# Optimization experiments

Measured on AMD Instinct MI355X. Metric: run time of the kernel, lower is better.

## Reference

```python
import jax, jax.numpy as jnp
import numpy as np

B, N, E, H, NDIM, WS = 1, 4096, 512, 8, 16, 128


def setup_inputs() -> dict:
    key = jax.random.key(0)
    ks = jax.random.split(key, 8)
    x = jax.random.normal(ks[0], (B, N, E), jnp.float32)
    W_qkv = jax.random.normal(ks[1], (E, 3 * E), jnp.float32) * (E ** -0.5)
    b_qkv = jnp.zeros((3 * E,), jnp.float32)
    W_out = jax.random.normal(ks[2], (E, E), jnp.float32) * (E ** -0.5)
    b_out = jnp.zeros((E,), jnp.float32)
    omega = jax.random.normal(ks[3], (E,), jnp.float32)
    p_coeff = 0.1 * jax.random.normal(ks[4], (E, NDIM), jnp.float32)
    # keep |q|<1 so the 4096-step EMA recurrence is stable (original randn init diverges)
    q_coeff = jax.random.uniform(ks[5], (E, NDIM), jnp.float32, minval=-0.95, maxval=0.95)
    gamma = 0.1 * jax.random.normal(ks[6], (E, NDIM), jnp.float32)
    adaptive_weights = jnp.ones((2,), jnp.float32)
    return dict(x=x, W_qkv=W_qkv, b_qkv=b_qkv, W_out=W_out, b_out=b_out,
                omega=omega, p_coeff=p_coeff, q_coeff=q_coeff, gamma=gamma,
                adaptive_weights=adaptive_weights)


def reference(x, W_qkv, b_qkv, W_out, b_out, omega, p_coeff, q_coeff, gamma, adaptive_weights):
    b, n, e = x.shape
    dk = e // H
    # qkv projection
    qkv = x @ W_qkv + b_qkv                                # (b, n, 3e)
    q, k, v = jnp.split(qkv, 3, axis=-1)
    to_heads = lambda t: t.reshape(b, n, H, dk).transpose(0, 2, 1, 3)  # (b, h, n, dk)
    q, k, v = to_heads(q), to_heads(k), to_heads(v)
    # full QK^T (as in source) then block-local causal multiplicative mask
    dots = jnp.einsum('bhid,bhjd->bhij', q, k) * (dk ** -0.5)
    idx = jnp.arange(n)
    blk, pos = idx // WS, idx % WS
    mask = (blk[:, None] == blk[None, :]) & (pos[None, :] <= pos[:, None])
    dots = dots * mask.astype(dots.dtype)                  # scores * tril within each window block, 0 elsewhere
    attn = jax.nn.softmax(dots, axis=-1)                   # dropout is identity in eval
    out_attn = jnp.einsum('bhij,bhjd->bhid', attn, v)
    out_attn = out_attn.transpose(0, 2, 1, 3).reshape(b, n, e) @ W_out + b_out
    # CEMA: per-channel linear recurrence h_t = p*x_t + q*h_{t-1}; y_t = sum_d gamma*h_t
    # (source uses complex64 hidden but p,q,gamma,x are real -> imag part stays 0; .real == real math)
    ndim = p_coeff.shape[1]
    def step(h, xt):                                       # h: (b, e, ndim), xt: (b, e)
        h = p_coeff[None] * xt[:, :, None] + q_coeff[None] * h
        return h, jnp.sum(gamma[None] * h, axis=-1)        # (b, e)
    h0 = jnp.zeros((b, e, ndim), x.dtype)
    _, ys = jax.lax.scan(step, h0, jnp.swapaxes(x, 0, 1))  # ys: (n, b, e)
    x_cema = jnp.swapaxes(ys, 0, 1)
    w = jax.nn.softmax(adaptive_weights)
    return w[0] * out_attn + w[1] * x_cema
```

## Files before the change

### kernel.cpp

```cpp
#include <hip/hip_runtime.h>
#include <hip/hip_bf16.h>


typedef __bf16 bf16x8 __attribute__((ext_vector_type(8)));
typedef float  f32x4  __attribute__((ext_vector_type(4)));

#define N_TOK   4096
#define EDIM    512
#define DKH     64
#define WSZ     128
#define QKV_LD  1536
#define CCH     128
#define CLEN    32

__device__ __forceinline__ void glds16(const void* gsrc, void* ldst) {
  __builtin_amdgcn_global_load_lds(
      (const __attribute__((address_space(1))) void*)gsrc,
      (__attribute__((address_space(3))) void*)ldst,
      16, 0, 0);
}

__global__ __launch_bounds__(256) void prep_weights(const float* __restrict__ Wq,
                                                    __bf16* __restrict__ WtQ,
                                                    const float* __restrict__ Wo,
                                                    __bf16* __restrict__ WtO) {
  __shared__ float tile[64][65];
  int bx = blockIdx.x;
  const int by = blockIdx.y, t = threadIdx.x;
  const float* in;
  __bf16* out;
  int C;
  if (bx < 24) { in = Wq; out = WtQ; C = 1536; }
  else         { bx -= 24; in = Wo; out = WtO; C = 512; }
  const int R = 512;
#pragma unroll
  for (int i = 0; i < 16; i++) {
    int idx = t + i * 256;
    int r = idx >> 6, c = idx & 63;
    tile[r][c] = in[(size_t)(by * 64 + r) * C + bx * 64 + c];
  }
  __syncthreads();
#pragma unroll
  for (int i = 0; i < 16; i++) {
    int idx = t + i * 256;
    int r = idx >> 6, c = idx & 63;
    out[(size_t)(bx * 64 + r) * R + by * 64 + c] = (__bf16)tile[c][r];
  }
}

__global__ __launch_bounds__(256) void vtot_kernel(const __bf16* __restrict__ WtQ,
                                                   const float* __restrict__ b_qkv,
                                                   const float* __restrict__ xsum,
                                                   float* __restrict__ vtot) {
  const int wid = threadIdx.x >> 6, lane = threadIdx.x & 63;
  const int c = blockIdx.x * 4 + wid;
  const bf16x8 wv = *(const bf16x8*)(WtQ + (size_t)(1024 + c) * 512 + lane * 8);
  const float4 x0 = *(const float4*)(xsum + lane * 8);
  const float4 x1 = *(const float4*)(xsum + lane * 8 + 4);
  float s = (float)wv[0] * x0.x + (float)wv[1] * x0.y + (float)wv[2] * x0.z + (float)wv[3] * x0.w
          + (float)wv[4] * x1.x + (float)wv[5] * x1.y + (float)wv[6] * x1.z + (float)wv[7] * x1.w;
#pragma unroll
  for (int m = 1; m < 64; m <<= 1) s += __shfl_xor(s, m);
  if (lane == 0) vtot[c] = s + (float)N_TOK * b_qkv[1024 + c];
}

template <int MODE, int BM, int BN, int WM, int WN>
__global__ __launch_bounds__(256) void gemm_bt(const __bf16* __restrict__ A,
                                               const __bf16* __restrict__ Bt,
                                               const float* __restrict__ bias,
                                               __bf16* __restrict__ Cb,
                                               float* __restrict__ Cf,
                                               int K, int ldc,
                                               const float* __restrict__ cema,
                                               const float* __restrict__ aw) {
  __shared__ __bf16 As[BM * 32];
  __shared__ __bf16 Bs[BN * 32];
  const int t = threadIdx.x;
  const int lane = t & 63, wid = t >> 6;
  const int quad = lane >> 4, c16 = lane & 15;
  const int wm = (wid % (BM / WM)) * WM, wn = (wid / (BM / WM)) * WN;
  const int m0 = blockIdx.x * BM, n0 = blockIdx.y * BN;

  f32x4 acc[WM / 16][WN / 16] = {};

  const int ar = t >> 2, ac = (t & 3) * 8;
  const __bf16* gA = A + (size_t)(m0 + ar) * K + ac;
  const __bf16* gB = Bt + (size_t)(n0 + ar) * K + ac;

  for (int k0 = 0; k0 < K; k0 += 32) {
#pragma unroll
    for (int i = 0; i < BM / 64; i++)
      glds16(gA + (size_t)i * 64 * K + k0, As + i * 2048 + t * 8);
#pragma unroll
    for (int i = 0; i < BN / 64; i++)
      glds16(gB + (size_t)i * 64 * K + k0, Bs + i * 2048 + t * 8);
    __syncthreads();
    bf16x8 af[WM / 16], bf[WN / 16];
#pragma unroll
    for (int i = 0; i < WM / 16; i++)
      af[i] = *(const bf16x8*)&As[(wm + i * 16 + c16) * 32 + quad * 8];
#pragma unroll
    for (int i = 0; i < WN / 16; i++)
      bf[i] = *(const bf16x8*)&Bs[(wn + i * 16 + c16) * 32 + quad * 8];
#pragma unroll
    for (int mi = 0; mi < WM / 16; mi++)
#pragma unroll
      for (int ni = 0; ni < WN / 16; ni++)
        acc[mi][ni] = __builtin_amdgcn_mfma_f32_16x16x32_bf16(af[mi], bf[ni], acc[mi][ni], 0, 0, 0);
    __syncthreads();
  }

  float w0 = 1.f, w1 = 0.f;
  if (MODE == 1) {
    float a0 = aw[0], a1 = aw[1];
    float mx = fmaxf(a0, a1);
    float e0 = __expf(a0 - mx), e1 = __expf(a1 - mx);
    w0 = e0 / (e0 + e1);
    w1 = 1.f - w0;
  }
#pragma unroll
  for (int mi = 0; mi < WM / 16; mi++) {
#pragma unroll
    for (int ni = 0; ni < WN / 16; ni++) {
      const int col = n0 + wn + ni * 16 + c16;
      const float bv = bias[col];
#pragma unroll
      for (int r = 0; r < 4; r++) {
        const int row = m0 + wm + mi * 16 + quad * 4 + r;
        float v = acc[mi][ni][r] + bv;
        if (MODE == 1) {
          v = w0 * v + w1 * cema[(size_t)row * EDIM + col];
          Cf[(size_t)row * ldc + col] = v;
        } else {
          Cb[(size_t)row * ldc + col] = (__bf16)v;
        }
      }
    }
  }
}

__global__ __launch_bounds__(256) void attn_kernel(const __bf16* __restrict__ qkv,
                                                   const float* __restrict__ vtot,
                                                   __bf16* __restrict__ out_attn) {
  __shared__ float4 smem4[3104];
  __bf16* Qs = (__bf16*)smem4;
  __bf16* Ks = (__bf16*)smem4 + 8192;
  __bf16* Ws = (__bf16*)smem4;
  __bf16* Vt = (__bf16*)smem4 + 16384;
  float* rowsum = (float*)((__bf16*)smem4 + 24576);

  const int t = threadIdx.x;
  const int lane = t & 63, wid = t >> 6;
  const int quad = lane >> 4, c16 = lane & 15;
  const int h = blockIdx.x & 7, w = blockIdx.x >> 3;
  const size_t base = (size_t)w * WSZ * QKV_LD + h * DKH;

  const int sr = t >> 3, sc = (t & 7) * 8;
#pragma unroll
  for (int i = 0; i < 4; i++) {
    glds16(qkv + base + (size_t)(i * 32 + sr) * QKV_LD + sc,        Qs + i * 2048 + t * 8);
    glds16(qkv + base + EDIM + (size_t)(i * 32 + sr) * QKV_LD + sc, Ks + i * 2048 + t * 8);
  }
  __syncthreads();

  const int wm = (wid & 1) * 64, wn = (wid >> 1) * 64;
  f32x4 accs[4][4] = {};
#pragma unroll
  for (int k0 = 0; k0 < DKH; k0 += 32) {
    bf16x8 af[4], bf[4];
#pragma unroll
    for (int i = 0; i < 4; i++) {
      af[i] = *(const bf16x8*)&Qs[(wm + i * 16 + c16) * DKH + k0 + quad * 8];
      bf[i] = *(const bf16x8*)&Ks[(wn + i * 16 + c16) * DKH + k0 + quad * 8];
    }
#pragma unroll
    for (int mi = 0; mi < 4; mi++)
#pragma unroll
      for (int ni = 0; ni < 4; ni++)
        accs[mi][ni] = __builtin_amdgcn_mfma_f32_16x16x32_bf16(af[mi], bf[ni], accs[mi][ni], 0, 0, 0);
  }
  __syncthreads();

  if (t < 128) rowsum[t] = 0.f;
  __syncthreads();

#pragma unroll
  for (int mi = 0; mi < 4; mi++) {
    float rs[4] = {0.f, 0.f, 0.f, 0.f};
#pragma unroll
    for (int ni = 0; ni < 4; ni++) {
      const int j = wn + ni * 16 + c16;
#pragma unroll
      for (int r = 0; r < 4; r++) {
        const int i = wm + mi * 16 + quad * 4 + r;
        const float s = accs[mi][ni][r] * 0.125f;
        const float wv = (j <= i) ? (__expf(s) - 1.f) : 0.f;
        Ws[i * 128 + j] = (__bf16)wv;
        rs[r] += wv;
      }
    }
#pragma unroll
    for (int m = 1; m < 16; m <<= 1)
#pragma unroll
      for (int r = 0; r < 4; r++) rs[r] += __shfl_xor(rs[r], m);
    if (c16 == 0) {
#pragma unroll
      for (int r = 0; r < 4; r++)
        atomicAdd(&rowsum[wm + mi * 16 + quad * 4 + r], rs[r]);
    }
  }

  {
    const int j = t & 127;
    const int dh = (t >> 7) * 32;
    const __bf16* vp = qkv + base + 2 * EDIM + (size_t)j * QKV_LD + dh;
#pragma unroll
    for (int u = 0; u < 4; u++) {
      bf16x8 vv = *(const bf16x8*)(vp + u * 8);
#pragma unroll
      for (int x2 = 0; x2 < 8; x2++) Vt[(dh + u * 8 + x2) * 128 + j] = vv[x2];
    }
  }
  __syncthreads();

  f32x4 acco[2][4] = {};
#pragma unroll
  for (int j0 = 0; j0 < 128; j0 += 32) {
    bf16x8 af2[2], bf2[4];
#pragma unroll
    for (int mi = 0; mi < 2; mi++)
      af2[mi] = *(const bf16x8*)&Ws[(wid * 32 + mi * 16 + c16) * 128 + j0 + quad * 8];
#pragma unroll
    for (int ni = 0; ni < 4; ni++)
      bf2[ni] = *(const bf16x8*)&Vt[(ni * 16 + c16) * 128 + j0 + quad * 8];
#pragma unroll
    for (int mi = 0; mi < 2; mi++)
#pragma unroll
      for (int ni = 0; ni < 4; ni++)
        acco[mi][ni] = __builtin_amdgcn_mfma_f32_16x16x32_bf16(af2[mi], bf2[ni], acco[mi][ni], 0, 0, 0);
  }

#pragma unroll
  for (int mi = 0; mi < 2; mi++) {
#pragma unroll
    for (int ni = 0; ni < 4; ni++) {
      const int d = ni * 16 + c16;
      const float vt = vtot[h * DKH + d];
#pragma unroll
      for (int r = 0; r < 4; r++) {
        const int i = wid * 32 + mi * 16 + quad * 4 + r;
        const float denom = rowsum[i] + (float)N_TOK;
        const float val = (acco[mi][ni][r] + vt) / denom;
        out_attn[(size_t)(w * WSZ + i) * EDIM + h * DKH + d] = (__bf16)val;
      }
    }
  }
}

__global__ __launch_bounds__(512) void cema_passA(const float* __restrict__ x,
                                                  const float* __restrict__ p_coeff,
                                                  const float* __restrict__ q_coeff,
                                                  float* __restrict__ h_end,
                                                  __bf16* __restrict__ x_bf,
                                                  float* __restrict__ xsum) {
  const int c = blockIdx.x, e = threadIdx.x;
  float p[16], q[16], h[16];
#pragma unroll
  for (int d4 = 0; d4 < 4; d4++) {
    const float4 pv = ((const float4*)(p_coeff + e * 16))[d4];
    const float4 qv = ((const float4*)(q_coeff + e * 16))[d4];
    p[d4 * 4 + 0] = pv.x; p[d4 * 4 + 1] = pv.y; p[d4 * 4 + 2] = pv.z; p[d4 * 4 + 3] = pv.w;
    q[d4 * 4 + 0] = qv.x; q[d4 * 4 + 1] = qv.y; q[d4 * 4 + 2] = qv.z; q[d4 * 4 + 3] = qv.w;
  }
#pragma unroll
  for (int d = 0; d < 16; d++) h[d] = 0.f;
  const float* xp = x + (size_t)c * CLEN * EDIM + e;
  __bf16* xb = x_bf + (size_t)c * CLEN * EDIM + e;
  float sx = 0.f;
#pragma unroll 4
  for (int tt = 0; tt < CLEN; tt++) {
    const float xv = xp[(size_t)tt * EDIM];
    xb[(size_t)tt * EDIM] = (__bf16)xv;
    sx += xv;
#pragma unroll
    for (int d = 0; d < 16; d++) h[d] = fmaf(p[d], xv, q[d] * h[d]);
  }
  atomicAdd(&xsum[e], sx);
  float* o = h_end + (size_t)c * 8192 + e * 16;
#pragma unroll
  for (int d = 0; d < 16; d++) o[d] = h[d];
}

__global__ __launch_bounds__(256) void cema_passB1(const float* __restrict__ q_coeff,
                                                   const float* __restrict__ h_end,
                                                   float* __restrict__ hin_local,
                                                   float* __restrict__ T) {
  const int idx = blockIdx.x * 256 + threadIdx.x;
  const int g = idx >> 13;
  const int i = idx & 8191;
  const float q = q_coeff[i];
  float Q = q * q; Q = Q * Q; Q = Q * Q; Q = Q * Q; Q = Q * Q;
  float L = 0.f;
  const int c0 = g * 16;
#pragma unroll 4
  for (int j = 0; j < 16; j++) {
    hin_local[(size_t)(c0 + j) * 8192 + i] = L;
    L = h_end[(size_t)(c0 + j) * 8192 + i] + Q * L;
  }
  T[(size_t)g * 8192 + i] = L;
}

__global__ __launch_bounds__(256) void cema_passB2(const float* __restrict__ q_coeff,
                                                   const float* __restrict__ T,
                                                   float* __restrict__ S) {
  const int i = blockIdx.x * 256 + threadIdx.x;
  const float q = q_coeff[i];
  float Q = q * q; Q = Q * Q; Q = Q * Q; Q = Q * Q; Q = Q * Q;
  float Q16 = Q * Q; Q16 = Q16 * Q16; Q16 = Q16 * Q16; Q16 = Q16 * Q16;
  float Sv = 0.f;
#pragma unroll
  for (int g = 0; g < 8; g++) {
    S[(size_t)g * 8192 + i] = Sv;
    Sv = T[(size_t)g * 8192 + i] + Q16 * Sv;
  }
}

__global__ __launch_bounds__(512) void cema_passC(const float* __restrict__ x,
                                                  const float* __restrict__ p_coeff,
                                                  const float* __restrict__ q_coeff,
                                                  const float* __restrict__ gamma,
                                                  const float* __restrict__ hin_local,
                                                  const float* __restrict__ S,
                                                  float* __restrict__ y) {
  const int c = blockIdx.x, e = threadIdx.x;
  const int g = c >> 4, j = c & 15;
  float p[16], q[16], gm[16], h[16];
#pragma unroll
  for (int d4 = 0; d4 < 4; d4++) {
    const float4 pv = ((const float4*)(p_coeff + e * 16))[d4];
    const float4 qv = ((const float4*)(q_coeff + e * 16))[d4];
    const float4 gv = ((const float4*)(gamma + e * 16))[d4];
    p[d4 * 4 + 0] = pv.x; p[d4 * 4 + 1] = pv.y; p[d4 * 4 + 2] = pv.z; p[d4 * 4 + 3] = pv.w;
    q[d4 * 4 + 0] = qv.x; q[d4 * 4 + 1] = qv.y; q[d4 * 4 + 2] = qv.z; q[d4 * 4 + 3] = qv.w;
    gm[d4 * 4 + 0] = gv.x; gm[d4 * 4 + 1] = gv.y; gm[d4 * 4 + 2] = gv.z; gm[d4 * 4 + 3] = gv.w;
  }
  const float* hi = hin_local + (size_t)c * 8192 + e * 16;
  const float* Sg = S + (size_t)g * 8192 + e * 16;
#pragma unroll
  for (int d = 0; d < 16; d++) {
    float Qd = q[d] * q[d]; Qd = Qd * Qd; Qd = Qd * Qd; Qd = Qd * Qd; Qd = Qd * Qd;
    float Qj = 1.f;
    for (int jj = 0; jj < j; jj++) Qj *= Qd;
    h[d] = hi[d] + Qj * Sg[d];
  }
  const float* xp = x + (size_t)c * CLEN * EDIM + e;
  float* yp = y + (size_t)c * CLEN * EDIM + e;
#pragma unroll 4
  for (int tt = 0; tt < CLEN; tt++) {
    const float xv = xp[(size_t)tt * EDIM];
    float acc = 0.f;
#pragma unroll
    for (int d = 0; d < 16; d++) {
      h[d] = fmaf(p[d], xv, q[d] * h[d]);
      acc = fmaf(gm[d], h[d], acc);
    }
    yp[(size_t)tt * EDIM] = acc;
  }
}

extern "C" void kernel_launch(void* const* d_in, const int* in_sizes, int n_in,
                              void* d_out, int out_size, void* d_ws, size_t ws_size,
                              hipStream_t stream) {
  const float* x       = (const float*)d_in[0];
  const float* W_qkv   = (const float*)d_in[1];
  const float* b_qkv   = (const float*)d_in[2];
  const float* W_out   = (const float*)d_in[3];
  const float* b_out   = (const float*)d_in[4];
  const float* p_coeff = (const float*)d_in[6];
  const float* q_coeff = (const float*)d_in[7];
  const float* gamma   = (const float*)d_in[8];
  const float* aw      = (const float*)d_in[9];

  char* ws = (char*)d_ws;
  __bf16* qkv      = (__bf16*)(ws);
  __bf16* WtQ      = (__bf16*)(ws + 12582912);
  __bf16* WtO      = (__bf16*)(ws + 14155776);
  __bf16* out_attn = (__bf16*)(ws + 14680064);
  float*  vtot     = (float*) (ws + 18874368);
  float*  h_end    = (float*) (ws + 18876416);
  float*  hin      = (float*) (ws + 23070720);
  float*  y        = (float*) (ws + 27265024);
  __bf16* x_bf     = (__bf16*)(ws + 35653632);
  float*  xsum     = (float*) (ws + 39847936);
  float*  Tg       = (float*) (ws + 39849984);
  float*  Sg       = (float*) (ws + 40112128);

  (void)hipMemsetAsync(xsum, 0, 512 * sizeof(float), stream);

  prep_weights<<<dim3(32, 8), 256, 0, stream>>>(W_qkv, WtQ, W_out, WtO);

  cema_passA<<<CCH, 512, 0, stream>>>(x, p_coeff, q_coeff, h_end, x_bf, xsum);
  cema_passB1<<<256, 256, 0, stream>>>(q_coeff, h_end, hin, Tg);
  cema_passB2<<<32, 256, 0, stream>>>(q_coeff, Tg, Sg);
  cema_passC<<<CCH, 512, 0, stream>>>(x, p_coeff, q_coeff, gamma, hin, Sg, y);

  vtot_kernel<<<128, 256, 0, stream>>>(WtQ, b_qkv, xsum, vtot);

  gemm_bt<0, 128, 64, 64, 32><<<dim3(32, 24), 256, 0, stream>>>(
      x_bf, WtQ, b_qkv, qkv, nullptr, EDIM, QKV_LD, nullptr, nullptr);

  attn_kernel<<<256, 256, 0, stream>>>(qkv, vtot, out_attn);

  gemm_bt<1, 64, 64, 32, 32><<<dim3(64, 8), 256, 0, stream>>>(
      out_attn, WtO, b_out, nullptr, (float*)d_out, EDIM, EDIM, y, aw);
}
```

Baseline: 149.8 us.

## Merge independent stages into block-partitioned fused kernels to cut launch count

The change folds the weight transpose and CEMA pass A into one launch, the QKV GEMM, the CEMA chunk scan and the vtot reduction into a second, and attention plus CEMA pass C into a third. Pass B2 is removed: pass C now rebuilds the inter-group prefix serially from T using Q^512. CEMA passes now run 256-thread blocks over half the channels each. This cuts the launch count from nine kernels to four and lets independent work share the GPU concurrently. The cost is extra serial work in pass C and larger 128x128 GEMM tiles, which change occupancy.

New measurement: 127.5 us. 1.18x faster.

```diff
diff --git a/kernel.cpp b/kernel.cpp
--- a/kernel.cpp
+++ b/kernel.cpp
@@ -20,66 +20,22 @@
       16, 0, 0);
 }
 
-__global__ __launch_bounds__(256) void prep_weights(const float* __restrict__ Wq,
-                                                    __bf16* __restrict__ WtQ,
-                                                    const float* __restrict__ Wo,
-                                                    __bf16* __restrict__ WtO) {
-  __shared__ float tile[64][65];
-  int bx = blockIdx.x;
-  const int by = blockIdx.y, t = threadIdx.x;
-  const float* in;
-  __bf16* out;
-  int C;
-  if (bx < 24) { in = Wq; out = WtQ; C = 1536; }
-  else         { bx -= 24; in = Wo; out = WtO; C = 512; }
-  const int R = 512;
-#pragma unroll
-  for (int i = 0; i < 16; i++) {
-    int idx = t + i * 256;
-    int r = idx >> 6, c = idx & 63;
-    tile[r][c] = in[(size_t)(by * 64 + r) * C + bx * 64 + c];
-  }
-  __syncthreads();
-#pragma unroll
-  for (int i = 0; i < 16; i++) {
-    int idx = t + i * 256;
-    int r = idx >> 6, c = idx & 63;
-    out[(size_t)(bx * 64 + r) * R + by * 64 + c] = (__bf16)tile[c][r];
-  }
-}
-
-__global__ __launch_bounds__(256) void vtot_kernel(const __bf16* __restrict__ WtQ,
-                                                   const float* __restrict__ b_qkv,
-                                                   const float* __restrict__ xsum,
-                                                   float* __restrict__ vtot) {
-  const int wid = threadIdx.x >> 6, lane = threadIdx.x & 63;
-  const int c = blockIdx.x * 4 + wid;
-  const bf16x8 wv = *(const bf16x8*)(WtQ + (size_t)(1024 + c) * 512 + lane * 8);
-  const float4 x0 = *(const float4*)(xsum + lane * 8);
-  const float4 x1 = *(const float4*)(xsum + lane * 8 + 4);
-  float s = (float)wv[0] * x0.x + (float)wv[1] * x0.y + (float)wv[2] * x0.z + (float)wv[3] * x0.w
-          + (float)wv[4] * x1.x + (float)wv[5] * x1.y + (float)wv[6] * x1.z + (float)wv[7] * x1.w;
-#pragma unroll
-  for (int m = 1; m < 64; m <<= 1) s += __shfl_xor(s, m);
-  if (lane == 0) vtot[c] = s + (float)N_TOK * b_qkv[1024 + c];
-}
-
 template <int MODE, int BM, int BN, int WM, int WN>
-__global__ __launch_bounds__(256) void gemm_bt(const __bf16* __restrict__ A,
-                                               const __bf16* __restrict__ Bt,
-                                               const float* __restrict__ bias,
-                                               __bf16* __restrict__ Cb,
-                                               float* __restrict__ Cf,
-                                               int K, int ldc,
-                                               const float* __restrict__ cema,
-                                               const float* __restrict__ aw) {
+__device__ __forceinline__ void gemm_body(const __bf16* __restrict__ A,
+                                          const __bf16* __restrict__ Bt,
+                                          const float* __restrict__ bias,
+                                          __bf16* __restrict__ Cb,
+                                          float* __restrict__ Cf,
+                                          int K, int ldc,
+                                          const float* __restrict__ cema,
+                                          const float* __restrict__ aw,
+                                          int bx, int by, int t) {
   __shared__ __bf16 As[BM * 32];
   __shared__ __bf16 Bs[BN * 32];
-  const int t = threadIdx.x;
   const int lane = t & 63, wid = t >> 6;
   const int quad = lane >> 4, c16 = lane & 15;
   const int wm = (wid % (BM / WM)) * WM, wn = (wid / (BM / WM)) * WN;
-  const int m0 = blockIdx.x * BM, n0 = blockIdx.y * BN;
+  const int m0 = bx * BM, n0 = by * BN;
 
   f32x4 acc[WM / 16][WN / 16] = {};
 
@@ -139,233 +95,298 @@
   }
 }
 
-__global__ __launch_bounds__(256) void attn_kernel(const __bf16* __restrict__ qkv,
-                                                   const float* __restrict__ vtot,
-                                                   __bf16* __restrict__ out_attn) {
-  __shared__ float4 smem4[3104];
-  __bf16* Qs = (__bf16*)smem4;
-  __bf16* Ks = (__bf16*)smem4 + 8192;
-  __bf16* Ws = (__bf16*)smem4;
-  __bf16* Vt = (__bf16*)smem4 + 16384;
-  float* rowsum = (float*)((__bf16*)smem4 + 24576);
-
-  const int t = threadIdx.x;
-  const int lane = t & 63, wid = t >> 6;
-  const int quad = lane >> 4, c16 = lane & 15;
-  const int h = blockIdx.x & 7, w = blockIdx.x >> 3;
-  const size_t base = (size_t)w * WSZ * QKV_LD + h * DKH;
-
-  const int sr = t >> 3, sc = (t & 7) * 8;
-#pragma unroll
-  for (int i = 0; i < 4; i++) {
-    glds16(qkv + base + (size_t)(i * 32 + sr) * QKV_LD + sc,        Qs + i * 2048 + t * 8);
-    glds16(qkv + base + EDIM + (size_t)(i * 32 + sr) * QKV_LD + sc, Ks + i * 2048 + t * 8);
-  }
-  __syncthreads();
-
-  const int wm = (wid & 1) * 64, wn = (wid >> 1) * 64;
-  f32x4 accs[4][4] = {};
-#pragma unroll
-  for (int k0 = 0; k0 < DKH; k0 += 32) {
-    bf16x8 af[4], bf[4];
+__global__ __launch_bounds__(256) void fused_prep_cemaA(const float* __restrict__ Wq,
+                                                        __bf16* __restrict__ WtQ,
+                                                        const float* __restrict__ Wo,
+                                                        __bf16* __restrict__ WtO,
+                                                        const float* __restrict__ x,
+                                                        const float* __restrict__ pc,
+                                                        const float* __restrict__ qc,
+                                                        float* __restrict__ h_end,
+                                                        __bf16* __restrict__ x_bf,
+                                                        float* __restrict__ xsum) {
+  const int b = blockIdx.x, t = threadIdx.x;
+  if (b < 256) {
+    __shared__ float tile[64][65];
+    int bx = b & 31;
+    const int by = b >> 5;
+    const float* in;
+    __bf16* out;
+    int C;
+    if (bx < 24) { in = Wq; out = WtQ; C = 1536; }
+    else         { bx -= 24; in = Wo; out = WtO; C = 512; }
+    const int R = 512;
+#pragma unroll
+    for (int i = 0; i < 16; i++) {
+      int idx = t + i * 256;
+      int r = idx >> 6, c = idx & 63;
+      tile[r][c] = in[(size_t)(by * 64 + r) * C + bx * 64 + c];
+    }
+    __syncthreads();
+#pragma unroll
+    for (int i = 0; i < 16; i++) {
+      int idx = t + i * 256;
+      int r = idx >> 6, c = idx & 63;
+      out[(size_t)(bx * 64 + r) * R + by * 64 + c] = (__bf16)tile[c][r];
+    }
+  } else {
+    const int bb = b - 256;
+    const int c = bb >> 1;
+    const int e = ((bb & 1) << 8) + t;
+    float p[16], q[16], h[16];
+#pragma unroll
+    for (int d4 = 0; d4 < 4; d4++) {
+      const float4 pv = ((const float4*)(pc + e * 16))[d4];
+      const float4 qv = ((const float4*)(qc + e * 16))[d4];
+      p[d4 * 4 + 0] = pv.x; p[d4 * 4 + 1] = pv.y; p[d4 * 4 + 2] = pv.z; p[d4 * 4 + 3] = pv.w;
+      q[d4 * 4 + 0] = qv.x; q[d4 * 4 + 1] = qv.y; q[d4 * 4 + 2] = qv.z; q[d4 * 4 + 3] = qv.w;
+    }
+#pragma unroll
+    for (int d = 0; d < 16; d++) h[d] = 0.f;
+    const float* xp = x + (size_t)c * CLEN * EDIM + e;
+    __bf16* xb = x_bf + (size_t)c * CLEN * EDIM + e;
+    float sx = 0.f;
+#pragma unroll 4
+    for (int tt = 0; tt < CLEN; tt++) {
+      const float xv = xp[(size_t)tt * EDIM];
+      xb[(size_t)tt * EDIM] = (__bf16)xv;
+      sx += xv;
+#pragma unroll
+      for (int d = 0; d < 16; d++) h[d] = fmaf(p[d], xv, q[d] * h[d]);
+    }
+    atomicAdd(&xsum[e], sx);
+    float* o = h_end + (size_t)c * 8192 + e * 16;
+#pragma unroll
+    for (int d = 0; d < 16; d++) o[d] = h[d];
+  }
+}
+
+__global__ __launch_bounds__(256) void fused_qkv_scan_vtot(const __bf16* __restrict__ x_bf,
+                                                           const __bf16* __restrict__ WtQ,
+                                                           const float* __restrict__ b_qkv,
+                                                           __bf16* __restrict__ qkv,
+                                                           const float* __restrict__ qc,
+                                                           const float* __restrict__ h_end,
+                                                           float* __restrict__ hin,
+                                                           float* __restrict__ T,
+                                                           const float* __restrict__ xsum,
+                                                           float* __restrict__ vtot) {
+  const int b = blockIdx.x, t = threadIdx.x;
+  if (b < 384) {
+    gemm_body<0, 128, 128, 64, 64>(x_bf, WtQ, b_qkv, qkv, nullptr,
+                                   EDIM, QKV_LD, nullptr, nullptr,
+                                   b & 31, b >> 5, t);
+  } else if (b < 640) {
+    const int idx = (b - 384) * 256 + t;
+    const int g = idx >> 13;
+    const int i = idx & 8191;
+    const float q = qc[i];
+    float Q = q * q; Q = Q * Q; Q = Q * Q; Q = Q * Q; Q = Q * Q;
+    float L = 0.f;
+    const int c0 = g * 16;
+#pragma unroll 4
+    for (int j = 0; j < 16; j++) {
+      hin[(size_t)(c0 + j) * 8192 + i] = L;
+      L = h_end[(size_t)(c0 + j) * 8192 + i] + Q * L;
+    }
+    T[(size_t)g * 8192 + i] = L;
+  } else {
+    const int wid = t >> 6, lane = t & 63;
+    const int c = (b - 640) * 4 + wid;
+    const bf16x8 wv = *(const bf16x8*)(WtQ + (size_t)(1024 + c) * 512 + lane * 8);
+    const float4 x0 = *(const float4*)(xsum + lane * 8);
+    const float4 x1 = *(const float4*)(xsum + lane * 8 + 4);
+    float s = (float)wv[0] * x0.x + (float)wv[1] * x0.y + (float)wv[2] * x0.z + (float)wv[3] * x0.w
+            + (float)wv[4] * x1.x + (float)wv[5] * x1.y + (float)wv[6] * x1.z + (float)wv[7] * x1.w;
+#pragma unroll
+    for (int m = 1; m < 64; m <<= 1) s += __shfl_xor(s, m);
+    if (lane == 0) vtot[c] = s + (float)N_TOK * b_qkv[1024 + c];
+  }
+}
+
+__global__ __launch_bounds__(256) void fused_attn_cemaC(const __bf16* __restrict__ qkv,
+                                                        const float* __restrict__ vtot,
+                                                        __bf16* __restrict__ out_attn,
+                                                        const float* __restrict__ x,
+                                                        const float* __restrict__ pc,
+                                                        const float* __restrict__ qc,
+                                                        const float* __restrict__ gma,
+                                                        const float* __restrict__ hin,
+                                                        const float* __restrict__ T,
+                                                        float* __restrict__ y) {
+  const int b = blockIdx.x, t = threadIdx.x;
+  if (b < 256) {
+    __shared__ float4 smem4[3104];
+    __bf16* Qs = (__bf16*)smem4;
+    __bf16* Ks = (__bf16*)smem4 + 8192;
+    __bf16* Ws = (__bf16*)smem4;
+    __bf16* Vt = (__bf16*)smem4 + 16384;
+    float* rowsum = (float*)((__bf16*)smem4 + 24576);
+
+    const int lane = t & 63, wid = t >> 6;
+    const int quad = lane >> 4, c16 = lane & 15;
+    const int h = b & 7, w = b >> 3;
+    const size_t base = (size_t)w * WSZ * QKV_LD + h * DKH;
+
+    const int sr = t >> 3, sc = (t & 7) * 8;
 #pragma unroll
     for (int i = 0; i < 4; i++) {
-      af[i] = *(const bf16x8*)&Qs[(wm + i * 16 + c16) * DKH + k0 + quad * 8];
-      bf[i] = *(const bf16x8*)&Ks[(wn + i * 16 + c16) * DKH + k0 + quad * 8];
-    }
-#pragma unroll
-    for (int mi = 0; mi < 4; mi++)
+      glds16(qkv + base + (size_t)(i * 32 + sr) * QKV_LD + sc,        Qs + i * 2048 + t * 8);
+      glds16(qkv + base + EDIM + (size_t)(i * 32 + sr) * QKV_LD + sc, Ks + i * 2048 + t * 8);
+    }
+    __syncthreads();
+
+    const int wm = (wid & 1) * 64, wn = (wid >> 1) * 64;
+    f32x4 accs[4][4] = {};
+#pragma unroll
+    for (int k0 = 0; k0 < DKH; k0 += 32) {
+      bf16x8 af[4], bf[4];
+#pragma unroll
+      for (int i = 0; i < 4; i++) {
+        af[i] = *(const bf16x8*)&Qs[(wm + i * 16 + c16) * DKH + k0 + quad * 8];
+        bf[i] = *(const bf16x8*)&Ks[(wn + i * 16 + c16) * DKH + k0 + quad * 8];
+      }
+#pragma unroll
+      for (int mi = 0; mi < 4; mi++)
+#pragma unroll
+        for (int ni = 0; ni < 4; ni++)
+          accs[mi][ni] = __builtin_amdgcn_mfma_f32_16x16x32_bf16(af[mi], bf[ni], accs[mi][ni], 0, 0, 0);
+    }
+    __syncthreads();
+
+    if (t < 128) rowsum[t] = 0.f;
+    __syncthreads();
+
+#pragma unroll
+    for (int mi = 0; mi < 4; mi++) {
+      float rs[4] = {0.f, 0.f, 0.f, 0.f};
+#pragma unroll
+      for (int ni = 0; ni < 4; ni++) {
+        const int j = wn + ni * 16 + c16;
+#pragma unroll
+        for (int r = 0; r < 4; r++) {
+          const int i = wm + mi * 16 + quad * 4 + r;
+          const float s = accs[mi][ni][r] * 0.125f;
+          const float wv = (j <= i) ? (__expf(s) - 1.f) : 0.f;
+          Ws[i * 128 + j] = (__bf16)wv;
+          rs[r] += wv;
+        }
+      }
+#pragma unroll
+      for (int m = 1; m < 16; m <<= 1)
+#pragma unroll
+        for (int r = 0; r < 4; r++) rs[r] += __shfl_xor(rs[r], m);
+      if (c16 == 0) {
+#pragma unroll
+        for (int r = 0; r < 4; r++)
+          atomicAdd(&rowsum[wm + mi * 16 + quad * 4 + r], rs[r]);
+      }
+    }
+
+    {
+      const int j = t & 127;
+      const int dh = (t >> 7) * 32;
+      const __bf16* vp = qkv + base + 2 * EDIM + (size_t)j * QKV_LD + dh;
+#pragma unroll
+      for (int u = 0; u < 4; u++) {
+        bf16x8 vv = *(const bf16x8*)(vp + u * 8);
+#pragma unroll
+        for (int x2 = 0; x2 < 8; x2++) Vt[(dh + u * 8 + x2) * 128 + j] = vv[x2];
+      }
+    }
+    __syncthreads();
+
+    f32x4 acco[2][4] = {};
+#pragma unroll
+    for (int j0 = 0; j0 < 128; j0 += 32) {
+      bf16x8 af2[2], bf2[4];
+#pragma unroll
+      for (int mi = 0; mi < 2; mi++)
+        af2[mi] = *(const bf16x8*)&Ws[(wid * 32 + mi * 16 + c16) * 128 + j0 + quad * 8];
 #pragma unroll
       for (int ni = 0; ni < 4; ni++)
-        accs[mi][ni] = __builtin_amdgcn_mfma_f32_16x16x32_bf16(af[mi], bf[ni], accs[mi][ni], 0, 0, 0);
-  }
-  __syncthreads();
-
-  if (t < 128) rowsum[t] = 0.f;
-  __syncthreads();
-
-#pragma unroll
-  for (int mi = 0; mi < 4; mi++) {
-    float rs[4] = {0.f, 0.f, 0.f, 0.f};
-#pragma unroll
-    for (int ni = 0; ni < 4; ni++) {
-      const int j = wn + ni * 16 + c16;
-#pragma unroll
-      for (int r = 0; r < 4; r++) {
-        const int i = wm + mi * 16 + quad * 4 + r;
-        const float s = accs[mi][ni][r] * 0.125f;
-        const float wv = (j <= i) ? (__expf(s) - 1.f) : 0.f;
-        Ws[i * 128 + j] = (__bf16)wv;
-        rs[r] += wv;
-      }
-    }
-#pragma unroll
-    for (int m = 1; m < 16; m <<= 1)
-#pragma unroll
-      for (int r = 0; r < 4; r++) rs[r] += __shfl_xor(rs[r], m);
-    if (c16 == 0) {
-#pragma unroll
-      for (int r = 0; r < 4; r++)
-        atomicAdd(&rowsum[wm + mi * 16 + quad * 4 + r], rs[r]);
-    }
-  }
-
-  {
-    const int j = t & 127;
-    const int dh = (t >> 7) * 32;
-    const __bf16* vp = qkv + base + 2 * EDIM + (size_t)j * QKV_LD + dh;
-#pragma unroll
-    for (int u = 0; u < 4; u++) {
-      bf16x8 vv = *(const bf16x8*)(vp + u * 8);
-#pragma unroll
-      for (int x2 = 0; x2 < 8; x2++) Vt[(dh + u * 8 + x2) * 128 + j] = vv[x2];
-    }
-  }
-  __syncthreads();
-
-  f32x4 acco[2][4] = {};
-#pragma unroll
-  for (int j0 = 0; j0 < 128; j0 += 32) {
-    bf16x8 af2[2], bf2[4];
-#pragma unroll
-    for (int mi = 0; mi < 2; mi++)
-      af2[mi] = *(const bf16x8*)&Ws[(wid * 32 + mi * 16 + c16) * 128 + j0 + quad * 8];
-#pragma unroll
-    for (int ni = 0; ni < 4; ni++)
-      bf2[ni] = *(const bf16x8*)&Vt[(ni * 16 + c16) * 128 + j0 + quad * 8];
-#pragma unroll
-    for (int mi = 0; mi < 2; mi++)
-#pragma unroll
-      for (int ni = 0; ni < 4; ni++)
-        acco[mi][ni] = __builtin_amdgcn_mfma_f32_16x16x32_bf16(af2[mi], bf2[ni], acco[mi][ni], 0, 0, 0);
-  }
-
-#pragma unroll
-  for (int mi = 0; mi < 2; mi++) {
-#pragma unroll
-    for (int ni = 0; ni < 4; ni++) {
-      const int d = ni * 16 + c16;
-      const float vt = vtot[h * DKH + d];
-#pragma unroll
-      for (int r = 0; r < 4; r++) {
-        const int i = wid * 32 + mi * 16 + quad * 4 + r;
-        const float denom = rowsum[i] + (float)N_TOK;
-        const float val = (acco[mi][ni][r] + vt) / denom;
-        out_attn[(size_t)(w * WSZ + i) * EDIM + h * DKH + d] = (__bf16)val;
-      }
-    }
-  }
-}
-
-__global__ __launch_bounds__(512) void cema_passA(const float* __restrict__ x,
-                                                  const float* __restrict__ p_coeff,
-                                                  const float* __restrict__ q_coeff,
-                                                  float* __restrict__ h_end,
-                                                  __bf16* __restrict__ x_bf,
-                                                  float* __restrict__ xsum) {
-  const int c = blockIdx.x, e = threadIdx.x;
-  float p[16], q[16], h[16];
-#pragma unroll
-  for (int d4 = 0; d4 < 4; d4++) {
-    const float4 pv = ((const float4*)(p_coeff + e * 16))[d4];
-    const float4 qv = ((const float4*)(q_coeff + e * 16))[d4];
-    p[d4 * 4 + 0] = pv.x; p[d4 * 4 + 1] = pv.y; p[d4 * 4 + 2] = pv.z; p[d4 * 4 + 3] = pv.w;
-    q[d4 * 4 + 0] = qv.x; q[d4 * 4 + 1] = qv.y; q[d4 * 4 + 2] = qv.z; q[d4 * 4 + 3] = qv.w;
-  }
-#pragma unroll
-  for (int d = 0; d < 16; d++) h[d] = 0.f;
-  const float* xp = x + (size_t)c * CLEN * EDIM + e;
-  __bf16* xb = x_bf + (size_t)c * CLEN * EDIM + e;
-  float sx = 0.f;
+        bf2[ni] = *(const bf16x8*)&Vt[(ni * 16 + c16) * 128 + j0 + quad * 8];
+#pragma unroll
+      for (int mi = 0; mi < 2; mi++)
+#pragma unroll
+        for (int ni = 0; ni < 4; ni++)
+          acco[mi][ni] = __builtin_amdgcn_mfma_f32_16x16x32_bf16(af2[mi], bf2[ni], acco[mi][ni], 0, 0, 0);
+    }
+
+#pragma unroll
+    for (int mi = 0; mi < 2; mi++) {
+#pragma unroll
+      for (int ni = 0; ni < 4; ni++) {
+        const int d = ni * 16 + c16;
+        const float vt = vtot[h * DKH + d];
+#pragma unroll
+        for (int r = 0; r < 4; r++) {
+          const int i = wid * 32 + mi * 16 + quad * 4 + r;
+          const float denom = rowsum[i] + (float)N_TOK;
+          const float val = (acco[mi][ni][r] + vt) / denom;
+          out_attn[(size_t)(w * WSZ + i) * EDIM + h * DKH + d] = (__bf16)val;
+        }
+      }
+    }
+  } else {
+    const int bb = b - 256;
+    const int c = bb >> 1;
+    const int e = ((bb & 1) << 8) + t;
+    const int g = c >> 4, j = c & 15;
+    float p[16], q[16], gm[16], h[16], Sv[16], Q32[16], Q512[16];
+#pragma unroll
+    for (int d4 = 0; d4 < 4; d4++) {
+      const float4 pv = ((const float4*)(pc + e * 16))[d4];
+      const float4 qv = ((const float4*)(qc + e * 16))[d4];
+      const float4 gv = ((const float4*)(gma + e * 16))[d4];
+      p[d4 * 4 + 0] = pv.x; p[d4 * 4 + 1] = pv.y; p[d4 * 4 + 2] = pv.z; p[d4 * 4 + 3] = pv.w;
+      q[d4 * 4 + 0] = qv.x; q[d4 * 4 + 1] = qv.y; q[d4 * 4 + 2] = qv.z; q[d4 * 4 + 3] = qv.w;
+      gm[d4 * 4 + 0] = gv.x; gm[d4 * 4 + 1] = gv.y; gm[d4 * 4 + 2] = gv.z; gm[d4 * 4 + 3] = gv.w;
+    }
+#pragma unroll
+    for (int d = 0; d < 16; d++) {
+      float Q = q[d] * q[d]; Q = Q * Q; Q = Q * Q; Q = Q * Q; Q = Q * Q;
+      Q32[d] = Q;
+      float Q5 = Q * Q; Q5 = Q5 * Q5; Q5 = Q5 * Q5; Q5 = Q5 * Q5;
+      Q512[d] = Q5;
+      Sv[d] = 0.f;
+    }
+    for (int gg = 0; gg < g; gg++) {
+      const float* Tp = T + (size_t)gg * 8192 + e * 16;
+#pragma unroll
+      for (int d = 0; d < 16; d++) Sv[d] = Tp[d] + Q512[d] * Sv[d];
+    }
+    const float* hi = hin + (size_t)c * 8192 + e * 16;
+#pragma unroll
+    for (int d = 0; d < 16; d++) {
+      float Qj = 1.f;
+      for (int jj = 0; jj < j; jj++) Qj *= Q32[d];
+      h[d] = hi[d] + Qj * Sv[d];
+    }
+    const float* xp = x + (size_t)c * CLEN * EDIM + e;
+    float* yp = y + (size_t)c * CLEN * EDIM + e;
 #pragma unroll 4
-  for (int tt = 0; tt < CLEN; tt++) {
-    const float xv = xp[(size_t)tt * EDIM];
-    xb[(size_t)tt * EDIM] = (__bf16)xv;
-    sx += xv;
-#pragma unroll
-    for (int d = 0; d < 16; d++) h[d] = fmaf(p[d], xv, q[d] * h[d]);
-  }
-  atomicAdd(&xsum[e], sx);
-  float* o = h_end + (size_t)c * 8192 + e * 16;
-#pragma unroll
-  for (int d = 0; d < 16; d++) o[d] = h[d];
-}
-
-__global__ __launch_bounds__(256) void cema_passB1(const float* __restrict__ q_coeff,
-                                                   const float* __restrict__ h_end,
-                                                   float* __restrict__ hin_local,
-                                                   float* __restrict__ T) {
-  const int idx = blockIdx.x * 256 + threadIdx.x;
-  const int g = idx >> 13;
-  const int i = idx & 8191;
-  const float q = q_coeff[i];
-  float Q = q * q; Q = Q * Q; Q = Q * Q; Q = Q * Q; Q = Q * Q;
-  float L = 0.f;
-  const int c0 = g * 16;
-#pragma unroll 4
-  for (int j = 0; j < 16; j++) {
-    hin_local[(size_t)(c0 + j) * 8192 + i] = L;
-    L = h_end[(size_t)(c0 + j) * 8192 + i] + Q * L;
-  }
-  T[(size_t)g * 8192 + i] = L;
-}
-
-__global__ __launch_bounds__(256) void cema_passB2(const float* __restrict__ q_coeff,
-                                                   const float* __restrict__ T,
-                                                   float* __restrict__ S) {
-  const int i = blockIdx.x * 256 + threadIdx.x;
-  const float q = q_coeff[i];
-  float Q = q * q; Q = Q * Q; Q = Q * Q; Q = Q * Q; Q = Q * Q;
-  float Q16 = Q * Q; Q16 = Q16 * Q16; Q16 = Q16 * Q16; Q16 = Q16 * Q16;
-  float Sv = 0.f;
-#pragma unroll
-  for (int g = 0; g < 8; g++) {
-    S[(size_t)g * 8192 + i] = Sv;
-    Sv = T[(size_t)g * 8192 + i] + Q16 * Sv;
-  }
-}
-
-__global__ __launch_bounds__(512) void cema_passC(const float* __restrict__ x,
-                                                  const float* __restrict__ p_coeff,
-                                                  const float* __restrict__ q_coeff,
-                                                  const float* __restrict__ gamma,
-                                                  const float* __restrict__ hin_local,
-                                                  const float* __restrict__ S,
-                                                  float* __restrict__ y) {
-  const int c = blockIdx.x, e = threadIdx.x;
-  const int g = c >> 4, j = c & 15;
-  float p[16], q[16], gm[16], h[16];
-#pragma unroll
-  for (int d4 = 0; d4 < 4; d4++) {
-    const float4 pv = ((const float4*)(p_coeff + e * 16))[d4];
-    const float4 qv = ((const float4*)(q_coeff + e * 16))[d4];
-    const float4 gv = ((const float4*)(gamma + e * 16))[d4];
-    p[d4 * 4 + 0] = pv.x; p[d4 * 4 + 1] = pv.y; p[d4 * 4 + 2] = pv.z; p[d4 * 4 + 3] = pv.w;
-    q[d4 * 4 + 0] = qv.x; q[d4 * 4 + 1] = qv.y; q[d4 * 4 + 2] = qv.z; q[d4 * 4 + 3] = qv.w;
-    gm[d4 * 4 + 0] = gv.x; gm[d4 * 4 + 1] = gv.y; gm[d4 * 4 + 2] = gv.z; gm[d4 * 4 + 3] = gv.w;
-  }
-  const float* hi = hin_local + (size_t)c * 8192 + e * 16;
-  const float* Sg = S + (size_t)g * 8192 + e * 16;
-#pragma unroll
-  for (int d = 0; d < 16; d++) {
-    float Qd = q[d] * q[d]; Qd = Qd * Qd; Qd = Qd * Qd; Qd = Qd * Qd; Qd = Qd * Qd;
-    float Qj = 1.f;
-    for (int jj = 0; jj < j; jj++) Qj *= Qd;
-    h[d] = hi[d] + Qj * Sg[d];
-  }
-  const float* xp = x + (size_t)c * CLEN * EDIM + e;
-  float* yp = y + (size_t)c * CLEN * EDIM + e;
-#pragma unroll 4
-  for (int tt = 0; tt < CLEN; tt++) {
-    const float xv = xp[(size_t)tt * EDIM];
-    float acc = 0.f;
-#pragma unroll
-    for (int d = 0; d < 16; d++) {
-      h[d] = fmaf(p[d], xv, q[d] * h[d]);
-      acc = fmaf(gm[d], h[d], acc);
-    }
-    yp[(size_t)tt * EDIM] = acc;
-  }
+    for (int tt = 0; tt < CLEN; tt++) {
+      const float xv = xp[(size_t)tt * EDIM];
+      float acc = 0.f;
+#pragma unroll
+      for (int d = 0; d < 16; d++) {
+        h[d] = fmaf(p[d], xv, q[d] * h[d]);
+        acc = fmaf(gm[d], h[d], acc);
+      }
+      yp[(size_t)tt * EDIM] = acc;
+    }
+  }
+}
+
+__global__ __launch_bounds__(256) void gemm_out_kernel(const __bf16* __restrict__ A,
+                                                       const __bf16* __restrict__ Bt,
+                                                       const float* __restrict__ bias,
+                                                       float* __restrict__ Cf,
+                                                       const float* __restrict__ cema,
+                                                       const float* __restrict__ aw) {
+  gemm_body<1, 64, 64, 32, 32>(A, Bt, bias, nullptr, Cf, EDIM, EDIM, cema, aw,
+                               blockIdx.x, blockIdx.y, threadIdx.x);
 }
 
 extern "C" void kernel_launch(void* const* d_in, const int* in_sizes, int n_in,
@@ -393,24 +414,18 @@
   __bf16* x_bf     = (__bf16*)(ws + 35653632);
   float*  xsum     = (float*) (ws + 39847936);
   float*  Tg       = (float*) (ws + 39849984);
-  float*  Sg       = (float*) (ws + 40112128);
 
   (void)hipMemsetAsync(xsum, 0, 512 * sizeof(float), stream);
 
-  prep_weights<<<dim3(32, 8), 256, 0, stream>>>(W_qkv, WtQ, W_out, WtO);
-
-  cema_passA<<<CCH, 512, 0, stream>>>(x, p_coeff, q_coeff, h_end, x_bf, xsum);
-  cema_passB1<<<256, 256, 0, stream>>>(q_coeff, h_end, hin, Tg);
-  cema_passB2<<<32, 256, 0, stream>>>(q_coeff, Tg, Sg);
-  cema_passC<<<CCH, 512, 0, stream>>>(x, p_coeff, q_coeff, gamma, hin, Sg, y);
-
-  vtot_kernel<<<128, 256, 0, stream>>>(WtQ, b_qkv, xsum, vtot);
-
-  gemm_bt<0, 128, 64, 64, 32><<<dim3(32, 24), 256, 0, stream>>>(
-      x_bf, WtQ, b_qkv, qkv, nullptr, EDIM, QKV_LD, nullptr, nullptr);
-
-  attn_kernel<<<256, 256, 0, stream>>>(qkv, vtot, out_attn);
-
-  gemm_bt<1, 64, 64, 32, 32><<<dim3(64, 8), 256, 0, stream>>>(
-      out_attn, WtO, b_out, nullptr, (float*)d_out, EDIM, EDIM, y, aw);
-}
+  fused_prep_cemaA<<<512, 256, 0, stream>>>(W_qkv, WtQ, W_out, WtO,
+                                            x, p_coeff, q_coeff, h_end, x_bf, xsum);
+
+  fused_qkv_scan_vtot<<<768, 256, 0, stream>>>(x_bf, WtQ, b_qkv, qkv,
+                                               q_coeff, h_end, hin, Tg, xsum, vtot);
+
+  fused_attn_cemaC<<<512, 256, 0, stream>>>(qkv, vtot, out_attn,
+                                            x, p_coeff, q_coeff, gamma, hin, Tg, y);
+
+  gemm_out_kernel<<<dim3(64, 8), 256, 0, stream>>>(out_attn, WtO, b_out,
+                                                   (float*)d_out, y, aw);
+}
```
